# Kernel optimization log

Hardware: AMD Instinct MI355X
Metric: run time of the kernel (lower is better)

Reference implementation:

```python
import jax, jax.numpy as jnp
import numpy as np

# Dims / scalars (from init_kwargs: m = int(T/dt), delta = dt, theta_star = threshold)
M = 50000
N = 500
DELTA = 0.001
GLEAK = 1.0
TAUS = 10.0
THETA_STAR = 1.0
SPIKE_PROB = 0.02  # sparse binary spike raster as produced by time2spike


def setup_inputs() -> dict:
    key = jax.random.key(0)
    k1, k2, k3 = jax.random.split(key, 3)
    # binary spike raster [m, n]
    spikes = (jax.random.uniform(k1, (M, N)) < SPIKE_PROB).astype(jnp.float32)
    # synapse weights ~ N(w_mean=0.01, 0.01)
    w = (0.01 + 0.01 * jax.random.normal(k2, (N,))).astype(jnp.float32)
    # reversal potentials: half excitatory (ex=5), half inhibitory (inh=-1), shuffled
    vrev = jnp.where(jax.random.uniform(k3, (N,)) < 0.5, 5.0, -1.0).astype(jnp.float32)
    return {"spikes": spikes, "w": w, "vrev": vrev}


def reference(spikes, w, vrev):
    dtype = spikes.dtype
    decay = jnp.exp(jnp.asarray(-1.0 / TAUS, dtype))

    # _compute_exp: exp_temp[i] = (exp_temp[i-1] + spikes[i-1]) * exp(-1/taus), exp_temp[0] = 0
    def exp_step(carry, s):
        nxt = (carry + s) * decay
        return nxt, nxt

    _, e_tail = jax.lax.scan(exp_step, jnp.zeros((N,), dtype), spikes[:-1])
    exp_temp = jnp.concatenate([jnp.zeros((1, N), dtype), e_tail], axis=0)  # [M, N]

    # Gsyn_pre = |w| * exp_temp ; Isyn_pre = Vrev * |w| * exp_temp.
    # Only their per-timestep sums over synapses enter the vtr recurrence,
    # so contract over n immediately instead of materializing [M, N] products.
    absw = jnp.abs(w)
    g_sum = exp_temp @ absw            # [M] = sum_j Gsyn_pre[i, j]
    i_sum = exp_temp @ (vrev * absw)   # [M] = sum_j Isyn_pre[i, j]
    a = DELTA * (GLEAK + g_sum)        # per-step leak+conductance factor
    b = DELTA * i_sum                  # per-step input drive

    # _computevtr: if vtr[i-1] < theta: vtr[i] = vtr[i-1]*(1 - a[i-1]) + b[i-1]
    # else vtr[i] stays 0 (state reset after threshold crossing), vtr[0] = 0.
    def vtr_step(v, ab):
        ai, bi = ab
        nxt = jnp.where(v < THETA_STAR, v * (1.0 - ai) + bi, jnp.asarray(0.0, dtype))
        return nxt, nxt

    _, v_tail = jax.lax.scan(vtr_step, jnp.asarray(0.0, dtype), (a[:-1], b[:-1]))
    vtr = jnp.concatenate([jnp.zeros((1,), dtype), v_tail])  # [M]
    return vtr
```

## Files before the change

kernel.cpp:

```cpp
#include <hip/hip_runtime.h>
#include <cmath>

namespace {
constexpr int NELEM  = 50000;
constexpr int NSYN   = 500;
constexpr int NQ4    = 125;
constexpr int T      = 1024;
constexpr int SBLK   = 49;
constexpr int SLOTS  = SBLK * T;
constexpr int CMAXC  = (NELEM - 1) >> 6;
constexpr int NCH_PAD = 784;
constexpr int MAXSEG = 4096;
constexpr int NGRP   = NELEM / 8;
constexpr double DELTA_D = 1.0e-3;
constexpr double THETA_D = 1.0;
constexpr float  DECAY_F = 0.90483741803595957311f;
}

struct WS {
    double2 pq[SLOTS];
    double  eAm[SLOTS], eAg[SLOTS], eAi[SLOTS];
    double  ePl[SLOTS], eQl[SLOTS];
    double  rarr[SLOTS];
    double  gAm[64], gAg[64], gAi[64];
    double  gEm[64], gEg[64], gEi[64];
    double  gPp[64], gPq[64];
    double  gEp[64], gEq[64];
    double  gmaxR[1024];
    double  gbndQ[MAXSEG];
    int     gbnd[MAXSEG];
    int     gnseg;
    int     pad;
    float   swv[SLOTS];
    float   iwv[SLOTS];
};

__global__ __launch_bounds__(256) void k_rowdot(
    const float* __restrict__ spikes,
    const float* __restrict__ w,
    const float* __restrict__ vrev,
    float* __restrict__ swv,
    float* __restrict__ iwv)
{
    const int lane = threadIdx.x & 63;
    const int wv   = threadIdx.x >> 6;
    const int rg   = blockIdx.x * 4 + wv;
    if (rg >= NGRP) return;
    const int row0 = rg * 8;

    const float4* __restrict__ w4 = reinterpret_cast<const float4*>(w);
    const float4* __restrict__ r4 = reinterpret_cast<const float4*>(vrev);
    const int j1 = lane;
    const int j2 = lane + 64;
    const bool has2 = (j2 < NQ4);
    float4 a1 = w4[j1], r1 = r4[j1];
    float4 aw1 = make_float4(fabsf(a1.x), fabsf(a1.y), fabsf(a1.z), fabsf(a1.w));
    float4 ar1 = make_float4(aw1.x * r1.x, aw1.y * r1.y, aw1.z * r1.z, aw1.w * r1.w);
    float4 aw2 = make_float4(0.f, 0.f, 0.f, 0.f), ar2 = aw2;
    if (has2) {
        float4 a2 = w4[j2], r2 = r4[j2];
        aw2 = make_float4(fabsf(a2.x), fabsf(a2.y), fabsf(a2.z), fabsf(a2.w));
        ar2 = make_float4(aw2.x * r2.x, aw2.y * r2.y, aw2.z * r2.z, aw2.w * r2.w);
    }

    float sp[8], ip[8];
#pragma unroll
    for (int r = 0; r < 8; ++r) {
        const float4* __restrict__ srow =
            reinterpret_cast<const float4*>(spikes + (size_t)(row0 + r) * NSYN);
        float4 s1 = srow[j1];
        float a = s1.x * aw1.x + s1.y * aw1.y + s1.z * aw1.z + s1.w * aw1.w;
        float b = s1.x * ar1.x + s1.y * ar1.y + s1.z * ar1.z + s1.w * ar1.w;
        if (has2) {
            float4 s2 = srow[j2];
            a += s2.x * aw2.x + s2.y * aw2.y + s2.z * aw2.z + s2.w * aw2.w;
            b += s2.x * ar2.x + s2.y * ar2.y + s2.z * ar2.z + s2.w * ar2.w;
        }
        sp[r] = a; ip[r] = b;
    }
#pragma unroll
    for (int d = 32; d > 0; d >>= 1) {
#pragma unroll
        for (int r = 0; r < 8; ++r) {
            sp[r] += __shfl_xor(sp[r], d);
            ip[r] += __shfl_xor(ip[r], d);
        }
    }
    if (lane == 0) {
        *reinterpret_cast<float4*>(swv + row0)     = make_float4(sp[0], sp[1], sp[2], sp[3]);
        *reinterpret_cast<float4*>(swv + row0 + 4) = make_float4(sp[4], sp[5], sp[6], sp[7]);
        *reinterpret_cast<float4*>(iwv + row0)     = make_float4(ip[0], ip[1], ip[2], ip[3]);
        *reinterpret_cast<float4*>(iwv + row0 + 4) = make_float4(ip[4], ip[5], ip[6], ip[7]);
    }
}

__global__ __launch_bounds__(1024) void k_scanA(const float* __restrict__ swv,
                                                const float* __restrict__ iwv,
                                                WS* __restrict__ ws)
{
    const int tid = threadIdx.x, lane = tid & 63, wv = tid >> 6, blk = blockIdx.x;
    const int idx = blk * T + tid;
    const bool live = (idx < NELEM);
    const double decay = (double)DECAY_F;
    __shared__ double s_a[16], s_b[16], s_c[16];

    double s = live ? (double)swv[idx] : 0.0;
    double t = live ? (double)iwv[idx] : 0.0;
    double m_in = live ? decay : 1.0;
    double g_in = live ? s * decay : 0.0;
    double i_in = live ? t * decay : 0.0;
#pragma unroll
    for (int d = 1; d < 64; d <<= 1) {
        double pm = __shfl_up(m_in, d);
        double pg = __shfl_up(g_in, d);
        double pi = __shfl_up(i_in, d);
        if (lane >= d) {
            g_in = m_in * pg + g_in;
            i_in = m_in * pi + i_in;
            m_in = pm * m_in;
        }
    }
    if (lane == 63) { s_a[wv] = m_in; s_b[wv] = g_in; s_c[wv] = i_in; }
    __syncthreads();
    if (wv == 0) {
        double wm = (lane < 16) ? s_a[lane] : 1.0;
        double wg = (lane < 16) ? s_b[lane] : 0.0;
        double wi = (lane < 16) ? s_c[lane] : 0.0;
#pragma unroll
        for (int d = 1; d < 16; d <<= 1) {
            double pm = __shfl_up(wm, d);
            double pg = __shfl_up(wg, d);
            double pi = __shfl_up(wi, d);
            if (lane >= d) {
                wg = wm * pg + wg;
                wi = wm * pi + wi;
                wm = pm * wm;
            }
        }
        if (lane < 16) { s_a[lane] = wm; s_b[lane] = wg; s_c[lane] = wi; }
        if (lane == 15) { ws->gAm[blk] = wm; ws->gAg[blk] = wg; ws->gAi[blk] = wi; }
    }
    __syncthreads();
    double em = __shfl_up(m_in, 1), eg = __shfl_up(g_in, 1), ei = __shfl_up(i_in, 1);
    if (lane == 0) { em = 1.0; eg = 0.0; ei = 0.0; }
    if (wv > 0) {
        double qm = s_a[wv - 1], qg = s_b[wv - 1], qi = s_c[wv - 1];
        eg = em * qg + eg;
        ei = em * qi + ei;
        em = qm * em;
    }
    ws->eAm[idx] = em; ws->eAg[idx] = eg; ws->eAi[idx] = ei;
}

__global__ void k_aggA(WS* __restrict__ ws)
{
    const int lane = threadIdx.x;
    double am = (lane < SBLK) ? ws->gAm[lane] : 1.0;
    double ag = (lane < SBLK) ? ws->gAg[lane] : 0.0;
    double ai = (lane < SBLK) ? ws->gAi[lane] : 0.0;
#pragma unroll
    for (int d = 1; d < 64; d <<= 1) {
        double pm = __shfl_up(am, d);
        double pg = __shfl_up(ag, d);
        double pi = __shfl_up(ai, d);
        if (lane >= d) {
            ag = am * pg + ag;
            ai = am * pi + ai;
            am = pm * am;
        }
    }
    double em = __shfl_up(am, 1), eg = __shfl_up(ag, 1), ei = __shfl_up(ai, 1);
    if (lane == 0) { em = 1.0; eg = 0.0; ei = 0.0; }
    if (lane < SBLK) { ws->gEm[lane] = em; ws->gEg[lane] = eg; ws->gEi[lane] = ei; }
}

__global__ __launch_bounds__(1024) void k_scanB(WS* __restrict__ ws)
{
    const int tid = threadIdx.x, lane = tid & 63, wv = tid >> 6, blk = blockIdx.x;
    const int idx = blk * T + tid;
    const bool live = (idx < NELEM);
    __shared__ double s_a[16], s_b[16];

    double em = ws->eAm[idx], eg = ws->eAg[idx], ei = ws->eAi[idx];
    double qm = ws->gEm[blk], qg = ws->gEg[blk], qi = ws->gEi[blk];
    double Eg = em * qg + eg;
    double Ei = em * qi + ei;
    (void)qm;

    double p_in = 1.0, q_in = 0.0;
    if (live) {
        double aa = DELTA_D * (1.0 + Eg);
        double om = 1.0 - aa;
        p_in = om;
        q_in = (DELTA_D * Ei) / om;
    }
#pragma unroll
    for (int d = 1; d < 64; d <<= 1) {
        double pp = __shfl_up(p_in, d);
        double pq = __shfl_up(q_in, d);
        if (lane >= d) {
            q_in = pq + q_in / pp;
            p_in = pp * p_in;
        }
    }
    if (lane == 63) { s_a[wv] = p_in; s_b[wv] = q_in; }
    __syncthreads();
    if (wv == 0) {
        double wp = (lane < 16) ? s_a[lane] : 1.0;
        double wq = (lane < 16) ? s_b[lane] : 0.0;
#pragma unroll
        for (int d = 1; d < 16; d <<= 1) {
            double pp = __shfl_up(wp, d);
            double pq = __shfl_up(wq, d);
            if (lane >= d) {
                wq = pq + wq / pp;
                wp = pp * wp;
            }
        }
        if (lane < 16) { s_a[lane] = wp; s_b[lane] = wq; }
        if (lane == 15) { ws->gPp[blk] = wp; ws->gPq[blk] = wq; }
    }
    __syncthreads();
    double ep = __shfl_up(p_in, 1), eq = __shfl_up(q_in, 1);
    if (lane == 0) { ep = 1.0; eq = 0.0; }
    if (wv > 0) {
        double ap = s_a[wv - 1], aq = s_b[wv - 1];
        eq = aq + eq / ap;
        ep = ap * ep;
    }
    ws->ePl[idx] = ep; ws->eQl[idx] = eq;
}

__global__ void k_aggB(WS* __restrict__ ws)
{
    const int lane = threadIdx.x;
    double ap = (lane < SBLK) ? ws->gPp[lane] : 1.0;
    double aq = (lane < SBLK) ? ws->gPq[lane] : 0.0;
#pragma unroll
    for (int d = 1; d < 64; d <<= 1) {
        double pp = __shfl_up(ap, d);
        double pq = __shfl_up(aq, d);
        if (lane >= d) {
            aq = pq + aq / pp;
            ap = pp * ap;
        }
    }
    double ep = __shfl_up(ap, 1), eq = __shfl_up(aq, 1);
    if (lane == 0) { ep = 1.0; eq = 0.0; }
    if (lane < SBLK) { ws->gEp[lane] = ep; ws->gEq[lane] = eq; }
}

__global__ __launch_bounds__(1024) void k_apply(WS* __restrict__ ws)
{
    const int tid = threadIdx.x, lane = tid & 63, blk = blockIdx.x;
    const int idx = blk * T + tid;
    const bool live = (idx < NELEM);

    double pl = ws->ePl[idx], ql = ws->eQl[idx];
    double ap = ws->gEp[blk], aq = ws->gEq[blk];
    double Q = aq + ql / ap;
    double P = ap * pl;
    ws->pq[idx] = make_double2(P, Q);
    double R = live ? (Q - THETA_D / P) : -1.0e308;
    ws->rarr[idx] = R;
    double mR = R;
#pragma unroll
    for (int d = 32; d > 0; d >>= 1) mR = fmax(mR, __shfl_xor(mR, d));
    if (lane == 0) ws->gmaxR[idx >> 6] = mR;
}

__global__ __launch_bounds__(1024) void k_search(WS* __restrict__ ws)
{
    const int tid = threadIdx.x;
    __shared__ double smax[NCH_PAD];
    __shared__ double s_guard;

    for (int c = tid; c < NCH_PAD; c += T)
        smax[c] = (c <= CMAXC) ? ws->gmaxR[c] : -1.0e308;
    double acc = 0.0;
    for (int i = tid; i < NELEM; i += T) acc += ws->rarr[i];
    for (int i = tid; i < NELEM; i += T) acc += ws->pq[i].y;
    if (acc == -1.2345e300) s_guard = acc;
    __syncthreads();

    if (tid < 64) {
        const int lane = tid;
        int nseg = 1;
        if (lane == 0) { ws->gbnd[0] = 0; ws->gbndQ[0] = 0.0; }
        double Qr = 0.0;
        int pos = 1;
        while (pos < NELEM && nseg < MAXSEG) {
            int c = pos >> 6;
            int i0 = -1;
            while (true) {
                int cf = -1;
                for (int cb = c; cb <= CMAXC; cb += 64) {
                    int cc = cb + lane;
                    bool qy = (cc <= CMAXC) && (smax[cc] >= Qr);
                    unsigned long long m = __ballot(qy);
                    if (m) { cf = cb + __builtin_ctzll(m); break; }
                }
                if (cf < 0) break;
                int i = (cf << 6) + lane;
                bool valid = (i >= pos) && (i < NELEM);
                double rv = valid ? ws->rarr[i] : -1.0e308;
                unsigned long long m2 = __ballot(valid && (rv >= Qr));
                if (m2) { i0 = (cf << 6) + __builtin_ctzll(m2); break; }
                c = cf + 1;
                if (c > CMAXC) break;
            }
            if (i0 < 0) break;
            int nb = i0 + 1;
            if (nb >= NELEM) break;
            Qr = ws->pq[nb].y;
            if (lane == 0) { ws->gbnd[nseg] = nb; ws->gbndQ[nseg] = Qr; }
            nseg++;
            pos = nb + 1;
        }
        if (lane == 0) ws->gnseg = nseg;
    }
}

__global__ __launch_bounds__(1024) void k_fill(const WS* __restrict__ ws,
                                               float* __restrict__ out)
{
    __shared__ int    sb[MAXSEG];
    __shared__ double sq[MAXSEG];
    __shared__ int    s_nseg;
    const int tid = threadIdx.x;
    if (tid == 0) s_nseg = ws->gnseg;
    __syncthreads();
    const int nseg = s_nseg;
    for (int i = tid; i < nseg; i += T) { sb[i] = ws->gbnd[i]; sq[i] = ws->gbndQ[i]; }
    __syncthreads();

    const int idx = blockIdx.x * T + tid;
    if (idx < NELEM) {
        int lo = 0, hi = nseg - 1;
        while (lo < hi) {
            int mid = (lo + hi + 1) >> 1;
            if (sb[mid] <= idx) lo = mid; else hi = mid - 1;
        }
        if (idx == sb[lo]) {
            out[idx] = 0.0f;
        } else {
            double2 pl = ws->pq[idx];
            out[idx] = (float)(pl.x * (pl.y - sq[lo]));
        }
    }
}

extern "C" void kernel_launch(void* const* d_in, const int* in_sizes, int n_in,
                              void* d_out, int out_size, void* d_ws, size_t ws_size,
                              hipStream_t stream) {
    const float* spikes = (const float*)d_in[0];
    const float* w      = (const float*)d_in[1];
    const float* vrev   = (const float*)d_in[2];
    float* out = (float*)d_out;
    WS* ws = (WS*)d_ws;

    hipLaunchKernelGGL(k_rowdot, dim3((NGRP + 3) / 4), dim3(256), 0, stream,
                       spikes, w, vrev, ws->swv, ws->iwv);
    hipLaunchKernelGGL(k_scanA,  dim3(SBLK), dim3(T),  0, stream, ws->swv, ws->iwv, ws);
    hipLaunchKernelGGL(k_aggA,   dim3(1),    dim3(64), 0, stream, ws);
    hipLaunchKernelGGL(k_scanB,  dim3(SBLK), dim3(T),  0, stream, ws);
    hipLaunchKernelGGL(k_aggB,   dim3(1),    dim3(64), 0, stream, ws);
    hipLaunchKernelGGL(k_apply,  dim3(SBLK), dim3(T),  0, stream, ws);
    hipLaunchKernelGGL(k_search, dim3(1),    dim3(T),  0, stream, ws);
    hipLaunchKernelGGL(k_fill,   dim3(SBLK), dim3(T),  0, stream, ws, out);
}
```

Baseline: 203.2 us.

## Fuse scan, aggregate, search and fill stages into one cooperative kernel

Replaces seven small kernels (two block scans, two single-wave aggregations, apply, search, fill) with one cooperative-launch kernel that uses grid-wide syncs. Each block redoes the 49-entry cross-block aggregation itself, keeps the per-element prefix values in registers instead of writing and re-reading them, and packs R and Q into a single double2 array. The search reads the next Q from the same ballot load through a shuffle, and the other blocks prefetch rq into cache while the search runs. The cost is grid.sync overhead and a cooperative launch that needs all 49 large blocks resident at once.

```diff
diff --git a/kernel.cpp b/kernel.cpp
--- a/kernel.cpp
+++ b/kernel.cpp
@@ -1,5 +1,8 @@
 #include <hip/hip_runtime.h>
+#include <hip/hip_cooperative_groups.h>
 #include <cmath>
+
+namespace cg = cooperative_groups;
 
 namespace {
 constexpr int NELEM  = 50000;
@@ -18,14 +21,9 @@
 }
 
 struct WS {
-    double2 pq[SLOTS];
-    double  eAm[SLOTS], eAg[SLOTS], eAi[SLOTS];
-    double  ePl[SLOTS], eQl[SLOTS];
-    double  rarr[SLOTS];
+    double2 rq[SLOTS];
     double  gAm[64], gAg[64], gAi[64];
-    double  gEm[64], gEg[64], gEi[64];
     double  gPp[64], gPq[64];
-    double  gEp[64], gEq[64];
     double  gmaxR[1024];
     double  gbndQ[MAXSEG];
     int     gbnd[MAXSEG];
@@ -94,18 +92,23 @@
     }
 }
 
-__global__ __launch_bounds__(1024) void k_scanA(const float* __restrict__ swv,
-                                                const float* __restrict__ iwv,
-                                                WS* __restrict__ ws)
+__global__ __launch_bounds__(1024) void k_fused(WS* __restrict__ ws, float* __restrict__ out)
 {
+    cg::grid_group grid = cg::this_grid();
     const int tid = threadIdx.x, lane = tid & 63, wv = tid >> 6, blk = blockIdx.x;
     const int idx = blk * T + tid;
     const bool live = (idx < NELEM);
     const double decay = (double)DECAY_F;
+
     __shared__ double s_a[16], s_b[16], s_c[16];
-
-    double s = live ? (double)swv[idx] : 0.0;
-    double t = live ? (double)iwv[idx] : 0.0;
+    __shared__ double s_qg0, s_qi0, s_qp0, s_qq0;
+    __shared__ double smax[NCH_PAD];
+    __shared__ int    sb[MAXSEG];
+    __shared__ double sq[MAXSEG];
+    __shared__ int    s_nseg;
+
+    double s = live ? (double)ws->swv[idx] : 0.0;
+    double t = live ? (double)ws->iwv[idx] : 0.0;
     double m_in = live ? decay : 1.0;
     double g_in = live ? s * decay : 0.0;
     double i_in = live ? t * decay : 0.0;
@@ -149,44 +152,32 @@
         ei = em * qi + ei;
         em = qm * em;
     }
-    ws->eAm[idx] = em; ws->eAg[idx] = eg; ws->eAi[idx] = ei;
-}
-
-__global__ void k_aggA(WS* __restrict__ ws)
-{
-    const int lane = threadIdx.x;
-    double am = (lane < SBLK) ? ws->gAm[lane] : 1.0;
-    double ag = (lane < SBLK) ? ws->gAg[lane] : 0.0;
-    double ai = (lane < SBLK) ? ws->gAi[lane] : 0.0;
-#pragma unroll
-    for (int d = 1; d < 64; d <<= 1) {
-        double pm = __shfl_up(am, d);
-        double pg = __shfl_up(ag, d);
-        double pi = __shfl_up(ai, d);
-        if (lane >= d) {
-            ag = am * pg + ag;
-            ai = am * pi + ai;
-            am = pm * am;
-        }
-    }
-    double em = __shfl_up(am, 1), eg = __shfl_up(ag, 1), ei = __shfl_up(ai, 1);
-    if (lane == 0) { em = 1.0; eg = 0.0; ei = 0.0; }
-    if (lane < SBLK) { ws->gEm[lane] = em; ws->gEg[lane] = eg; ws->gEi[lane] = ei; }
-}
-
-__global__ __launch_bounds__(1024) void k_scanB(WS* __restrict__ ws)
-{
-    const int tid = threadIdx.x, lane = tid & 63, wv = tid >> 6, blk = blockIdx.x;
-    const int idx = blk * T + tid;
-    const bool live = (idx < NELEM);
-    __shared__ double s_a[16], s_b[16];
-
-    double em = ws->eAm[idx], eg = ws->eAg[idx], ei = ws->eAi[idx];
-    double qm = ws->gEm[blk], qg = ws->gEg[blk], qi = ws->gEi[blk];
-    double Eg = em * qg + eg;
-    double Ei = em * qi + ei;
-    (void)qm;
-
+
+    grid.sync();
+
+    if (wv == 0) {
+        double am = (lane < SBLK) ? ws->gAm[lane] : 1.0;
+        double ag = (lane < SBLK) ? ws->gAg[lane] : 0.0;
+        double ai = (lane < SBLK) ? ws->gAi[lane] : 0.0;
+#pragma unroll
+        for (int d = 1; d < 64; d <<= 1) {
+            double pm = __shfl_up(am, d);
+            double pg = __shfl_up(ag, d);
+            double pi = __shfl_up(ai, d);
+            if (lane >= d) {
+                ag = am * pg + ag;
+                ai = am * pi + ai;
+                am = pm * am;
+            }
+        }
+        double zg = __shfl_up(ag, 1), zi = __shfl_up(ai, 1);
+        if (lane == 0) { zg = 0.0; zi = 0.0; }
+        if (lane == blk) { s_qg0 = zg; s_qi0 = zi; }
+    }
+    __syncthreads();
+
+    double Eg = em * s_qg0 + eg;
+    double Ei = em * s_qi0 + ei;
     double p_in = 1.0, q_in = 0.0;
     if (live) {
         double aa = DELTA_D * (1.0 + Eg);
@@ -224,129 +215,112 @@
     double ep = __shfl_up(p_in, 1), eq = __shfl_up(q_in, 1);
     if (lane == 0) { ep = 1.0; eq = 0.0; }
     if (wv > 0) {
-        double ap = s_a[wv - 1], aq = s_b[wv - 1];
-        eq = aq + eq / ap;
-        ep = ap * ep;
-    }
-    ws->ePl[idx] = ep; ws->eQl[idx] = eq;
-}
-
-__global__ void k_aggB(WS* __restrict__ ws)
-{
-    const int lane = threadIdx.x;
-    double ap = (lane < SBLK) ? ws->gPp[lane] : 1.0;
-    double aq = (lane < SBLK) ? ws->gPq[lane] : 0.0;
-#pragma unroll
-    for (int d = 1; d < 64; d <<= 1) {
-        double pp = __shfl_up(ap, d);
-        double pq = __shfl_up(aq, d);
-        if (lane >= d) {
-            aq = pq + aq / pp;
-            ap = pp * ap;
-        }
-    }
-    double ep = __shfl_up(ap, 1), eq = __shfl_up(aq, 1);
-    if (lane == 0) { ep = 1.0; eq = 0.0; }
-    if (lane < SBLK) { ws->gEp[lane] = ep; ws->gEq[lane] = eq; }
-}
-
-__global__ __launch_bounds__(1024) void k_apply(WS* __restrict__ ws)
-{
-    const int tid = threadIdx.x, lane = tid & 63, blk = blockIdx.x;
-    const int idx = blk * T + tid;
-    const bool live = (idx < NELEM);
-
-    double pl = ws->ePl[idx], ql = ws->eQl[idx];
-    double ap = ws->gEp[blk], aq = ws->gEq[blk];
-    double Q = aq + ql / ap;
-    double P = ap * pl;
-    ws->pq[idx] = make_double2(P, Q);
+        double ap2 = s_a[wv - 1], aq2 = s_b[wv - 1];
+        eq = aq2 + eq / ap2;
+        ep = ap2 * ep;
+    }
+
+    grid.sync();
+
+    if (wv == 0) {
+        double ap = (lane < SBLK) ? ws->gPp[lane] : 1.0;
+        double aq = (lane < SBLK) ? ws->gPq[lane] : 0.0;
+#pragma unroll
+        for (int d = 1; d < 64; d <<= 1) {
+            double pp = __shfl_up(ap, d);
+            double pq = __shfl_up(aq, d);
+            if (lane >= d) {
+                aq = pq + aq / pp;
+                ap = pp * ap;
+            }
+        }
+        double zp = __shfl_up(ap, 1), zq = __shfl_up(aq, 1);
+        if (lane == 0) { zp = 1.0; zq = 0.0; }
+        if (lane == blk) { s_qp0 = zp; s_qq0 = zq; }
+    }
+    __syncthreads();
+    double Q = s_qq0 + eq / s_qp0;
+    double P = s_qp0 * ep;
     double R = live ? (Q - THETA_D / P) : -1.0e308;
-    ws->rarr[idx] = R;
+    ws->rq[idx] = make_double2(R, Q);
     double mR = R;
 #pragma unroll
     for (int d = 32; d > 0; d >>= 1) mR = fmax(mR, __shfl_xor(mR, d));
     if (lane == 0) ws->gmaxR[idx >> 6] = mR;
-}
-
-__global__ __launch_bounds__(1024) void k_search(WS* __restrict__ ws)
-{
-    const int tid = threadIdx.x;
-    __shared__ double smax[NCH_PAD];
-    __shared__ double s_guard;
-
-    for (int c = tid; c < NCH_PAD; c += T)
-        smax[c] = (c <= CMAXC) ? ws->gmaxR[c] : -1.0e308;
-    double acc = 0.0;
-    for (int i = tid; i < NELEM; i += T) acc += ws->rarr[i];
-    for (int i = tid; i < NELEM; i += T) acc += ws->pq[i].y;
-    if (acc == -1.2345e300) s_guard = acc;
-    __syncthreads();
-
-    if (tid < 64) {
-        const int lane = tid;
-        int nseg = 1;
-        if (lane == 0) { ws->gbnd[0] = 0; ws->gbndQ[0] = 0.0; }
-        double Qr = 0.0;
-        int pos = 1;
-        while (pos < NELEM && nseg < MAXSEG) {
-            int c = pos >> 6;
-            int i0 = -1;
-            while (true) {
-                int cf = -1;
-                for (int cb = c; cb <= CMAXC; cb += 64) {
-                    int cc = cb + lane;
-                    bool qy = (cc <= CMAXC) && (smax[cc] >= Qr);
-                    unsigned long long m = __ballot(qy);
-                    if (m) { cf = cb + __builtin_ctzll(m); break; }
+
+    grid.sync();
+
+    if (blk == 0) {
+        for (int c = tid; c < NCH_PAD; c += T)
+            smax[c] = (c <= CMAXC) ? ws->gmaxR[c] : -1.0e308;
+        __syncthreads();
+        if (tid < 64) {
+            int nseg = 1;
+            if (lane == 0) { ws->gbnd[0] = 0; ws->gbndQ[0] = 0.0; }
+            double Qr = 0.0;
+            int pos = 1;
+            while (pos < NELEM && nseg < MAXSEG) {
+                int c = pos >> 6;
+                int i0 = -1;
+                double Qnb = 0.0;
+                while (true) {
+                    int cf = -1;
+                    for (int cb = c; cb <= CMAXC; cb += 64) {
+                        int cc = cb + lane;
+                        bool qy = (cc <= CMAXC) && (smax[cc] >= Qr);
+                        unsigned long long m = __ballot(qy);
+                        if (m) { cf = cb + __builtin_ctzll(m); break; }
+                    }
+                    if (cf < 0) break;
+                    int i = (cf << 6) + lane;
+                    bool valid = (i >= pos) && (i < NELEM);
+                    double2 rv = valid ? ws->rq[i] : make_double2(-1.0e308, 0.0);
+                    unsigned long long m2 = __ballot(valid && (rv.x >= Qr));
+                    if (m2) {
+                        int r = __builtin_ctzll(m2);
+                        i0 = (cf << 6) + r;
+                        if (r < 63) Qnb = __shfl(rv.y, r + 1);
+                        break;
+                    }
+                    c = cf + 1;
+                    if (c > CMAXC) break;
                 }
-                if (cf < 0) break;
-                int i = (cf << 6) + lane;
-                bool valid = (i >= pos) && (i < NELEM);
-                double rv = valid ? ws->rarr[i] : -1.0e308;
-                unsigned long long m2 = __ballot(valid && (rv >= Qr));
-                if (m2) { i0 = (cf << 6) + __builtin_ctzll(m2); break; }
-                c = cf + 1;
-                if (c > CMAXC) break;
-            }
-            if (i0 < 0) break;
-            int nb = i0 + 1;
-            if (nb >= NELEM) break;
-            Qr = ws->pq[nb].y;
-            if (lane == 0) { ws->gbnd[nseg] = nb; ws->gbndQ[nseg] = Qr; }
-            nseg++;
-            pos = nb + 1;
-        }
-        if (lane == 0) ws->gnseg = nseg;
-    }
-}
-
-__global__ __launch_bounds__(1024) void k_fill(const WS* __restrict__ ws,
-                                               float* __restrict__ out)
-{
-    __shared__ int    sb[MAXSEG];
-    __shared__ double sq[MAXSEG];
-    __shared__ int    s_nseg;
-    const int tid = threadIdx.x;
+                if (i0 < 0) break;
+                int nb = i0 + 1;
+                if (nb >= NELEM) break;
+                if ((i0 & 63) == 63) Qnb = ws->rq[nb].y;
+                Qr = Qnb;
+                if (lane == 0) { ws->gbnd[nseg] = nb; ws->gbndQ[nseg] = Qr; }
+                nseg++;
+                pos = nb + 1;
+            }
+            if (lane == 0) ws->gnseg = nseg;
+        } else {
+            double acc = 0.0;
+            for (int i = tid; i < NELEM; i += 7 * T) acc += ws->rq[i].x;
+            asm volatile("" :: "v"((float)acc));
+        }
+    } else if ((blk & 7) == 0) {
+        const int p = blk >> 3;
+        double acc = 0.0;
+        for (int i = p * T + tid; i < NELEM; i += 7 * T) acc += ws->rq[i].x;
+        asm volatile("" :: "v"((float)acc));
+    }
+
+    grid.sync();
+
     if (tid == 0) s_nseg = ws->gnseg;
     __syncthreads();
     const int nseg = s_nseg;
-    for (int i = tid; i < nseg; i += T) { sb[i] = ws->gbnd[i]; sq[i] = ws->gbndQ[i]; }
-    __syncthreads();
-
-    const int idx = blockIdx.x * T + tid;
-    if (idx < NELEM) {
+    for (int i2 = tid; i2 < nseg; i2 += T) { sb[i2] = ws->gbnd[i2]; sq[i2] = ws->gbndQ[i2]; }
+    __syncthreads();
+    if (live) {
         int lo = 0, hi = nseg - 1;
         while (lo < hi) {
             int mid = (lo + hi + 1) >> 1;
             if (sb[mid] <= idx) lo = mid; else hi = mid - 1;
         }
-        if (idx == sb[lo]) {
-            out[idx] = 0.0f;
-        } else {
-            double2 pl = ws->pq[idx];
-            out[idx] = (float)(pl.x * (pl.y - sq[lo]));
-        }
+        out[idx] = (idx == sb[lo]) ? 0.0f : (float)(P * (Q - sq[lo]));
     }
 }
 
@@ -361,11 +335,9 @@
 
     hipLaunchKernelGGL(k_rowdot, dim3((NGRP + 3) / 4), dim3(256), 0, stream,
                        spikes, w, vrev, ws->swv, ws->iwv);
-    hipLaunchKernelGGL(k_scanA,  dim3(SBLK), dim3(T),  0, stream, ws->swv, ws->iwv, ws);
-    hipLaunchKernelGGL(k_aggA,   dim3(1),    dim3(64), 0, stream, ws);
-    hipLaunchKernelGGL(k_scanB,  dim3(SBLK), dim3(T),  0, stream, ws);
-    hipLaunchKernelGGL(k_aggB,   dim3(1),    dim3(64), 0, stream, ws);
-    hipLaunchKernelGGL(k_apply,  dim3(SBLK), dim3(T),  0, stream, ws);
-    hipLaunchKernelGGL(k_search, dim3(1),    dim3(T),  0, stream, ws);
-    hipLaunchKernelGGL(k_fill,   dim3(SBLK), dim3(T),  0, stream, ws, out);
+
+    WS* wsp = ws; float* outp = out;
+    void* args[2] = { (void*)&wsp, (void*)&outp };
+    (void)hipLaunchCooperativeKernel((const void*)k_fused, dim3(SBLK), dim3(T),
+                                     args, 0, stream);
 }
```

Measured after the change: 234.2 us. +15.2%, slower.
